# Kernel optimization log

Measured on AMD Instinct MI355X. Metric: run time of the kernel, lower is better.

## Reference

```python
import jax, jax.numpy as jnp
import numpy as np

B, S, D_IN = 4, 2048, 1024
EMBED, HEADS = 1024, 16
HEAD_DIM = EMBED // HEADS


def setup_inputs() -> dict:
    key = jax.random.key(0)
    k1, k2, k3 = jax.random.split(key, 3)
    x = jax.random.normal(k1, (B, S, D_IN), dtype=jnp.float32)
    # xavier-uniform-ish init scales
    lim_qkv = float(np.sqrt(6.0 / (D_IN + 3 * EMBED)))
    lim_o = float(np.sqrt(6.0 / (EMBED + EMBED)))
    w_qkv = jax.random.uniform(k2, (3 * EMBED, D_IN), minval=-lim_qkv, maxval=lim_qkv, dtype=jnp.float32)
    b_qkv = jnp.zeros((3 * EMBED,), dtype=jnp.float32)
    w_o = jax.random.uniform(k3, (EMBED, EMBED), minval=-lim_o, maxval=lim_o, dtype=jnp.float32)
    b_o = jnp.zeros((EMBED,), dtype=jnp.float32)
    return {"x": x, "w_qkv": w_qkv, "b_qkv": b_qkv, "w_o": w_o, "b_o": b_o}


def reference(x, w_qkv, b_qkv, w_o, b_o):
    b, s, _ = x.shape
    qkv = jnp.einsum('bsi,oi->bso', x, w_qkv) + b_qkv            # (b, s, 3E)
    qkv = qkv.reshape(b, s, HEADS, 3 * HEAD_DIM).transpose(0, 2, 1, 3)  # (b, h, s, 3d)
    q, k, v = jnp.split(qkv, 3, axis=-1)                          # each (b, h, s, d)
    scale = 1.0 / jnp.sqrt(jnp.float32(HEAD_DIM))
    attn = jnp.einsum('bhqd,bhkd->bhqk', q, k) * scale            # (b, h, s, s)
    attn = jax.nn.softmax(attn, axis=-1)
    vals = jnp.einsum('bhqk,bhkd->bhqd', attn, v)                 # (b, h, s, d)
    # NOTE: original torch code reshapes (b,h,s,d) -> (b,s,e) WITHOUT transposing
    # heads back; jnp.reshape reproduces that flattening exactly.
    vals = vals.reshape(b, s, EMBED)
    out = jnp.einsum('bse,oe->bso', vals, w_o) + b_o              # (b, s, E)
    return out
```

## Files before the change

### kernel.cpp

```cpp
#include <hip/hip_runtime.h>
#include <stdint.h>
#include <stddef.h>

#define DEVINL __device__ __forceinline__

typedef unsigned short u16;
typedef unsigned int u32;
typedef __attribute__((ext_vector_type(8))) short short8;
typedef __attribute__((ext_vector_type(4))) float f32x4;
typedef __attribute__((ext_vector_type(4))) u32 u32x4;
typedef __attribute__((ext_vector_type(2))) u32 u32x2;

#define QSCALE 0.18033688011112042f

DEVINL u16 f2bf(float f) {
    u32 u = __builtin_bit_cast(u32, f);
    u32 r = (u + 0x7fffu + ((u >> 16) & 1u)) >> 16;
    return (u16)r;
}

DEVINL void gld_lds16(const void* g, void* l) {
    __builtin_amdgcn_global_load_lds(
        (__attribute__((address_space(1))) u32*)(uintptr_t)g,
        (__attribute__((address_space(3))) u32*)l, 16, 0, 0);
}

DEVINL u32 pack_bf16_trunc(float lo, float hi) {
    return __builtin_amdgcn_perm(__builtin_bit_cast(u32, hi),
                                 __builtin_bit_cast(u32, lo), 0x07060302u);
}

__global__ void prep_inputs(const float* __restrict__ x, const float* __restrict__ wqkv,
                            const float* __restrict__ bqkv, const float* __restrict__ wo,
                            u16* __restrict__ xb, u16* __restrict__ wqb,
                            u16* __restrict__ wob, float* __restrict__ bsc) {
    int blk = blockIdx.x;
    if (blk < 6144) {
        const float* src; u16* dst; int base; bool qscale = false;
        if (blk < 4096)      { src = x;    dst = xb;  base = blk; }
        else if (blk < 5632) { src = wqkv; dst = wqb; base = blk - 4096; qscale = true; }
        else                 { src = wo;   dst = wob; base = blk - 5632; }
        int i = (base * 256 + threadIdx.x) * 8;
        float sc = 1.0f;
        if (qscale) { int row = i >> 10; if ((row % 192) < 64) sc = QSCALE; }
        float4 a = *(const float4*)(src + i);
        float4 c = *(const float4*)(src + i + 4);
        union { u16 s[8]; u32x4 v; } t;
        t.s[0] = f2bf(a.x * sc); t.s[1] = f2bf(a.y * sc); t.s[2] = f2bf(a.z * sc); t.s[3] = f2bf(a.w * sc);
        t.s[4] = f2bf(c.x * sc); t.s[5] = f2bf(c.y * sc); t.s[6] = f2bf(c.z * sc); t.s[7] = f2bf(c.w * sc);
        *(u32x4*)(dst + i) = t.v;
    } else {
        int i = (blk - 6144) * 256 + threadIdx.x;
        float sc = ((i % 192) < 64) ? QSCALE : 1.0f;
        bsc[i] = bqkv[i] * sc;
    }
}

__global__ void gemm_qkv(const u16* __restrict__ A, const u16* __restrict__ Bm,
                         const float* __restrict__ bias, u16* __restrict__ qkvb,
                         u16* __restrict__ vtb) {
    const int K = 1024, N = 3072;
    __shared__ u16 As[128 * 32];
    __shared__ u16 Bs[128 * 32];
    const int tid = threadIdx.x;
    const int lane = tid & 63;
    const int wv = tid >> 6, wr = wv >> 1, wc = wv & 1;
    const int l15 = lane & 15, quad = lane >> 4;
    const int m0 = blockIdx.y * 128, n0 = blockIdx.x * 128;

    f32x4 acc[4][4];
#pragma unroll
    for (int i = 0; i < 4; i++)
#pragma unroll
        for (int j = 0; j < 4; j++) acc[i][j] = (f32x4){0.f, 0.f, 0.f, 0.f};

    const u16* Ab = A + (size_t)m0 * K;
    const u16* Bb = Bm + (size_t)n0 * K;
    const int srow = tid >> 2;
    const int sc8 = (tid & 3) * 8;

    for (int k0 = 0; k0 < K; k0 += 32) {
#pragma unroll
        for (int i = 0; i < 2; i++) {
            int row = i * 64 + srow;
            gld_lds16(Ab + (size_t)row * K + k0 + sc8, (char*)As + (size_t)(i * 256 + tid) * 16);
            gld_lds16(Bb + (size_t)row * K + k0 + sc8, (char*)Bs + (size_t)(i * 256 + tid) * 16);
        }
        __syncthreads();
        short8 af[4], bf8[4];
#pragma unroll
        for (int mi = 0; mi < 4; mi++)
            af[mi] = *(const short8*)(As + (wr * 64 + mi * 16 + l15) * 32 + quad * 8);
#pragma unroll
        for (int ni = 0; ni < 4; ni++)
            bf8[ni] = *(const short8*)(Bs + (wc * 64 + ni * 16 + l15) * 32 + quad * 8);
#pragma unroll
        for (int mi = 0; mi < 4; mi++)
#pragma unroll
            for (int ni = 0; ni < 4; ni++)
                acc[mi][ni] = __builtin_amdgcn_mfma_f32_16x16x32_bf16(af[mi], bf8[ni], acc[mi][ni], 0, 0, 0);
        __syncthreads();
    }

#pragma unroll
    for (int mi = 0; mi < 4; mi++) {
        int row_b = m0 + wr * 64 + mi * 16 + quad * 4;
#pragma unroll
        for (int ni = 0; ni < 4; ni++) {
            int c0 = n0 + wc * 64 + ni * 16;
            int sec0 = c0 % 192;
            float bv = bias[c0 + l15];
            float v0 = acc[mi][ni][0] + bv;
            float v1 = acc[mi][ni][1] + bv;
            float v2 = acc[mi][ni][2] + bv;
            float v3 = acc[mi][ni][3] + bv;
            if (sec0 >= 128) {
                int hh = c0 / 192;
                int b = row_b >> 11;
                int s = row_b & 2047;
                int d = sec0 - 128 + l15;
                u32 lo = (u32)f2bf(v0) | ((u32)f2bf(v1) << 16);
                u32 hi = (u32)f2bf(v2) | ((u32)f2bf(v3) << 16);
                *(u32x2*)(vtb + ((size_t)((b * 16 + hh) * 64 + d)) * 2048 + s) = (u32x2){lo, hi};
            } else {
                int col = c0 + l15;
                qkvb[(size_t)(row_b + 0) * N + col] = f2bf(v0);
                qkvb[(size_t)(row_b + 1) * N + col] = f2bf(v1);
                qkvb[(size_t)(row_b + 2) * N + col] = f2bf(v2);
                qkvb[(size_t)(row_b + 3) * N + col] = f2bf(v3);
            }
        }
    }
}

__global__ void gemm_out(const u16* __restrict__ A, const u16* __restrict__ Bm,
                         const float* __restrict__ bias, float* __restrict__ C) {
    const int K = 1024, N = 1024;
    __shared__ u16 As[128 * 32];
    __shared__ u16 Bs[64 * 32];
    const int tid = threadIdx.x;
    const int lane = tid & 63;
    const int wv = tid >> 6, wr = wv >> 1, wc = wv & 1;
    const int l15 = lane & 15, quad = lane >> 4;
    const int m0 = blockIdx.y * 128, n0 = blockIdx.x * 64;

    f32x4 acc[4][2];
#pragma unroll
    for (int i = 0; i < 4; i++)
#pragma unroll
        for (int j = 0; j < 2; j++) acc[i][j] = (f32x4){0.f, 0.f, 0.f, 0.f};

    const u16* Ab = A + (size_t)m0 * K;
    const u16* Bb = Bm + (size_t)n0 * K;
    const int srow = tid >> 2;
    const int sc8 = (tid & 3) * 8;

    for (int k0 = 0; k0 < K; k0 += 32) {
#pragma unroll
        for (int i = 0; i < 2; i++)
            gld_lds16(Ab + (size_t)(i * 64 + srow) * K + k0 + sc8, (char*)As + (size_t)(i * 256 + tid) * 16);
        gld_lds16(Bb + (size_t)srow * K + k0 + sc8, (char*)Bs + (size_t)tid * 16);
        __syncthreads();
        short8 af[4], bf8[2];
#pragma unroll
        for (int mi = 0; mi < 4; mi++)
            af[mi] = *(const short8*)(As + (wr * 64 + mi * 16 + l15) * 32 + quad * 8);
#pragma unroll
        for (int ni = 0; ni < 2; ni++)
            bf8[ni] = *(const short8*)(Bs + (wc * 32 + ni * 16 + l15) * 32 + quad * 8);
#pragma unroll
        for (int mi = 0; mi < 4; mi++)
#pragma unroll
            for (int ni = 0; ni < 2; ni++)
                acc[mi][ni] = __builtin_amdgcn_mfma_f32_16x16x32_bf16(af[mi], bf8[ni], acc[mi][ni], 0, 0, 0);
        __syncthreads();
    }

#pragma unroll
    for (int mi = 0; mi < 4; mi++) {
        int row_b = m0 + wr * 64 + mi * 16 + quad * 4;
#pragma unroll
        for (int ni = 0; ni < 2; ni++) {
            int col = n0 + wc * 32 + ni * 16 + l15;
            float bv = bias[col];
#pragma unroll
            for (int r = 0; r < 4; r++)
                C[(size_t)(row_b + r) * N + col] = acc[mi][ni][r] + bv;
        }
    }
}

__launch_bounds__(256, 4)
__global__ void flash_attn(const u16* __restrict__ qkv, const u16* __restrict__ vt,
                           u16* __restrict__ vals2) {
    __shared__ u16 Ks[64 * 72];
    __shared__ u16 Vts[64 * 72];
    __shared__ u16 Ps[4][32 * 72];

    const int tid = threadIdx.x;
    const int lane = tid & 63, wv = tid >> 6;
    const int l15 = lane & 15, quad = lane >> 4;
    const int s0 = blockIdx.x * 128;
    const int bh = blockIdx.y, b = bh >> 4, h = bh & 15;

    short8 qf[2][2];
    const u16* qbase = qkv + (size_t)(b * 2048 + s0 + wv * 32) * 3072 + h * 192;
#pragma unroll
    for (int qi = 0; qi < 2; qi++)
#pragma unroll
        for (int ks = 0; ks < 2; ks++)
            qf[qi][ks] = *(const short8*)(qbase + (size_t)(qi * 16 + l15) * 3072 + ks * 32 + quad * 8);

    f32x4 o_acc[2][4];
    f32x4 sum_acc[2];
#pragma unroll
    for (int qi = 0; qi < 2; qi++) {
        sum_acc[qi] = (f32x4){0.f, 0.f, 0.f, 0.f};
#pragma unroll
        for (int nd = 0; nd < 4; nd++) o_acc[qi][nd] = (f32x4){0.f, 0.f, 0.f, 0.f};
    }

    const u16* kg = qkv + (size_t)(b * 2048) * 3072 + h * 192 + 64;
    const u16* vg = vt + (size_t)bh * 64 * 2048;
    const int srow = tid >> 2;
    const int sc16 = (tid & 3) * 16;

    const short8 ones = (short8){0x3F80, 0x3F80, 0x3F80, 0x3F80, 0x3F80, 0x3F80, 0x3F80, 0x3F80};

    for (int kb = 0; kb < 2048; kb += 64) {
        __syncthreads();
        u32x4 k0 = *(const u32x4*)(kg + (size_t)(kb + srow) * 3072 + sc16);
        u32x4 k1 = *(const u32x4*)(kg + (size_t)(kb + srow) * 3072 + sc16 + 8);
        u32x4 v0 = *(const u32x4*)(vg + (size_t)srow * 2048 + kb + sc16);
        u32x4 v1 = *(const u32x4*)(vg + (size_t)srow * 2048 + kb + sc16 + 8);
        *(u32x4*)(Ks + srow * 72 + sc16) = k0;
        *(u32x4*)(Ks + srow * 72 + sc16 + 8) = k1;
        *(u32x4*)(Vts + srow * 72 + sc16) = v0;
        *(u32x4*)(Vts + srow * 72 + sc16 + 8) = v1;
        __syncthreads();

        f32x4 s_acc[4][2];
#pragma unroll
        for (int ki = 0; ki < 4; ki++)
#pragma unroll
            for (int qi = 0; qi < 2; qi++) s_acc[ki][qi] = (f32x4){0.f, 0.f, 0.f, 0.f};
#pragma unroll
        for (int ki = 0; ki < 4; ki++) {
#pragma unroll
            for (int ks = 0; ks < 2; ks++) {
                short8 kf = *(const short8*)(Ks + (ki * 16 + l15) * 72 + ks * 32 + quad * 8);
#pragma unroll
                for (int qi = 0; qi < 2; qi++)
                    s_acc[ki][qi] = __builtin_amdgcn_mfma_f32_16x16x32_bf16(kf, qf[qi][ks], s_acc[ki][qi], 0, 0, 0);
            }
        }

#pragma unroll
        for (int ki = 0; ki < 4; ki++)
#pragma unroll
            for (int qi = 0; qi < 2; qi++) {
                float p0 = __builtin_amdgcn_exp2f(s_acc[ki][qi][0]);
                float p1 = __builtin_amdgcn_exp2f(s_acc[ki][qi][1]);
                float p2 = __builtin_amdgcn_exp2f(s_acc[ki][qi][2]);
                float p3 = __builtin_amdgcn_exp2f(s_acc[ki][qi][3]);
                u32x2 pk = (u32x2){pack_bf16_trunc(p0, p1), pack_bf16_trunc(p2, p3)};
                *(u32x2*)(Ps[wv] + (qi * 16 + l15) * 72 + ki * 16 + quad * 4) = pk;
            }

#pragma unroll
        for (int c = 0; c < 2; c++) {
            short8 ap[2];
#pragma unroll
            for (int qi = 0; qi < 2; qi++)
                ap[qi] = *(const short8*)(Ps[wv] + (qi * 16 + l15) * 72 + c * 32 + quad * 8);
#pragma unroll
            for (int qi = 0; qi < 2; qi++)
                sum_acc[qi] = __builtin_amdgcn_mfma_f32_16x16x32_bf16(ap[qi], ones, sum_acc[qi], 0, 0, 0);
#pragma unroll
            for (int nd = 0; nd < 4; nd++) {
                short8 bv = *(const short8*)(Vts + (nd * 16 + l15) * 72 + c * 32 + quad * 8);
#pragma unroll
                for (int qi = 0; qi < 2; qi++)
                    o_acc[qi][nd] = __builtin_amdgcn_mfma_f32_16x16x32_bf16(ap[qi], bv, o_acc[qi][nd], 0, 0, 0);
            }
        }
    }

#pragma unroll
    for (int qi = 0; qi < 2; qi++) {
        f32x4 inv;
#pragma unroll
        for (int r = 0; r < 4; r++) inv[r] = 1.0f / sum_acc[qi][r];
#pragma unroll
        for (int nd = 0; nd < 4; nd++) {
            int d = nd * 16 + l15;
#pragma unroll
            for (int r = 0; r < 4; r++) {
                int s = s0 + wv * 32 + qi * 16 + quad * 4 + r;
                size_t row2 = (size_t)(b * 2048 + h * 128 + (s >> 4));
                int col2 = ((s & 15) << 6) + d;
                vals2[row2 * 1024 + col2] = f2bf(o_acc[qi][nd][r] * inv[r]);
            }
        }
    }
}

extern "C" void kernel_launch(void* const* d_in, const int* in_sizes, int n_in,
                              void* d_out, int out_size, void* d_ws, size_t ws_size,
                              hipStream_t stream) {
    (void)in_sizes; (void)n_in; (void)out_size; (void)ws_size;
    const float* x      = (const float*)d_in[0];
    const float* w_qkv  = (const float*)d_in[1];
    const float* b_qkv  = (const float*)d_in[2];
    const float* w_o    = (const float*)d_in[3];
    const float* b_o    = (const float*)d_in[4];
    float* out = (float*)d_out;

    char* ws = (char*)d_ws;
    u16* xb   = (u16*)(ws);
    u16* wqb  = (u16*)(ws + 16777216);
    u16* wob  = (u16*)(ws + 23068672);
    u16* qkvb = (u16*)(ws + 25165824);
    u16* vtb  = (u16*)(ws + 75497472);
    u16* v2b  = (u16*)(ws + 92274688);
    float* bsc = (float*)(ws + 92274688);

    prep_inputs<<<6156, 256, 0, stream>>>(x, w_qkv, b_qkv, w_o, xb, wqb, wob, bsc);

    gemm_qkv<<<dim3(24, 64), 256, 0, stream>>>(xb, wqb, bsc, qkvb, vtb);

    flash_attn<<<dim3(16, 64), 256, 0, stream>>>(qkvb, vtb, v2b);

    gemm_out<<<dim3(16, 64), 256, 0, stream>>>(v2b, wob, b_o, out);
}
```

Baseline: 274.5 us.

## Split flash attention waves across query and key halves with cross-wave reduction

Each block now processes 128 keys per iteration. Waves are arranged as 2 query groups × 2 key halves, and each wave handles 64 queries against 64 keys, so every K/V fragment read from LDS feeds twice as many MFMAs. At the end, the partial O and row sums from the two key-half waves are combined through shared memory before normalisation. The cost is a larger register footprint (launch bounds drop from 4 to 2 blocks per CU), more LDS per block, and an extra reduction step.

```diff
diff --git a/kernel.cpp b/kernel.cpp
--- a/kernel.cpp
+++ b/kernel.cpp
@@ -190,31 +190,33 @@
     }
 }
 
-__launch_bounds__(256, 4)
+__launch_bounds__(256, 2)
 __global__ void flash_attn(const u16* __restrict__ qkv, const u16* __restrict__ vt,
                            u16* __restrict__ vals2) {
-    __shared__ u16 Ks[64 * 72];
-    __shared__ u16 Vts[64 * 72];
-    __shared__ u16 Ps[4][32 * 72];
+    __shared__ u16 SM[36352];
+    u16* Ks  = SM;
+    u16* Vts = SM + 9216;
+    u16* Ps  = SM + 17920;
 
     const int tid = threadIdx.x;
     const int lane = tid & 63, wv = tid >> 6;
+    const int qw = wv >> 1, kw = wv & 1;
     const int l15 = lane & 15, quad = lane >> 4;
     const int s0 = blockIdx.x * 128;
     const int bh = blockIdx.y, b = bh >> 4, h = bh & 15;
 
-    short8 qf[2][2];
-    const u16* qbase = qkv + (size_t)(b * 2048 + s0 + wv * 32) * 3072 + h * 192;
-#pragma unroll
-    for (int qi = 0; qi < 2; qi++)
+    short8 qf[4][2];
+    const u16* qbase = qkv + (size_t)(b * 2048 + s0 + qw * 64) * 3072 + h * 192;
+#pragma unroll
+    for (int qi = 0; qi < 4; qi++)
 #pragma unroll
         for (int ks = 0; ks < 2; ks++)
             qf[qi][ks] = *(const short8*)(qbase + (size_t)(qi * 16 + l15) * 3072 + ks * 32 + quad * 8);
 
-    f32x4 o_acc[2][4];
-    f32x4 sum_acc[2];
-#pragma unroll
-    for (int qi = 0; qi < 2; qi++) {
+    f32x4 o_acc[4][4];
+    f32x4 sum_acc[4];
+#pragma unroll
+    for (int qi = 0; qi < 4; qi++) {
         sum_acc[qi] = (f32x4){0.f, 0.f, 0.f, 0.f};
 #pragma unroll
         for (int nd = 0; nd < 4; nd++) o_acc[qi][nd] = (f32x4){0.f, 0.f, 0.f, 0.f};
@@ -222,35 +224,45 @@
 
     const u16* kg = qkv + (size_t)(b * 2048) * 3072 + h * 192 + 64;
     const u16* vg = vt + (size_t)bh * 64 * 2048;
-    const int srow = tid >> 2;
-    const int sc16 = (tid & 3) * 16;
-
+
+    const int krow = tid >> 1, khalf = (tid & 1) * 32;
+    const int vrow = tid >> 2, vq4 = (tid & 3) * 32;
+
+    u16* Pw = Ps + wv * 64 * 72;
     const short8 ones = (short8){0x3F80, 0x3F80, 0x3F80, 0x3F80, 0x3F80, 0x3F80, 0x3F80, 0x3F80};
 
-    for (int kb = 0; kb < 2048; kb += 64) {
-        __syncthreads();
-        u32x4 k0 = *(const u32x4*)(kg + (size_t)(kb + srow) * 3072 + sc16);
-        u32x4 k1 = *(const u32x4*)(kg + (size_t)(kb + srow) * 3072 + sc16 + 8);
-        u32x4 v0 = *(const u32x4*)(vg + (size_t)srow * 2048 + kb + sc16);
-        u32x4 v1 = *(const u32x4*)(vg + (size_t)srow * 2048 + kb + sc16 + 8);
-        *(u32x4*)(Ks + srow * 72 + sc16) = k0;
-        *(u32x4*)(Ks + srow * 72 + sc16 + 8) = k1;
-        *(u32x4*)(Vts + srow * 72 + sc16) = v0;
-        *(u32x4*)(Vts + srow * 72 + sc16 + 8) = v1;
-        __syncthreads();
-
-        f32x4 s_acc[4][2];
+    for (int kb = 0; kb < 2048; kb += 128) {
+        __syncthreads();
+        const u16* kgr = kg + (size_t)(kb + krow) * 3072 + khalf;
+        const u16* vgr = vg + (size_t)vrow * 2048 + kb + vq4;
+        u32x4 ka = *(const u32x4*)(kgr);
+        u32x4 kb4 = *(const u32x4*)(kgr + 8);
+        u32x4 kc = *(const u32x4*)(kgr + 16);
+        u32x4 kd = *(const u32x4*)(kgr + 24);
+        u32x4 va = *(const u32x4*)(vgr);
+        u32x4 vb4 = *(const u32x4*)(vgr + 8);
+        u32x4 vc = *(const u32x4*)(vgr + 16);
+        u32x4 vd = *(const u32x4*)(vgr + 24);
+        u16* kdst = Ks + krow * 72 + khalf;
+        u16* vdst = Vts + vrow * 136 + vq4;
+        *(u32x4*)(kdst) = ka;  *(u32x4*)(kdst + 8) = kb4;
+        *(u32x4*)(kdst + 16) = kc; *(u32x4*)(kdst + 24) = kd;
+        *(u32x4*)(vdst) = va;  *(u32x4*)(vdst + 8) = vb4;
+        *(u32x4*)(vdst + 16) = vc; *(u32x4*)(vdst + 24) = vd;
+        __syncthreads();
+
+        f32x4 s_acc[4][4];
 #pragma unroll
         for (int ki = 0; ki < 4; ki++)
 #pragma unroll
-            for (int qi = 0; qi < 2; qi++) s_acc[ki][qi] = (f32x4){0.f, 0.f, 0.f, 0.f};
+            for (int qi = 0; qi < 4; qi++) s_acc[ki][qi] = (f32x4){0.f, 0.f, 0.f, 0.f};
 #pragma unroll
         for (int ki = 0; ki < 4; ki++) {
 #pragma unroll
             for (int ks = 0; ks < 2; ks++) {
-                short8 kf = *(const short8*)(Ks + (ki * 16 + l15) * 72 + ks * 32 + quad * 8);
-#pragma unroll
-                for (int qi = 0; qi < 2; qi++)
+                short8 kf = *(const short8*)(Ks + (kw * 64 + ki * 16 + l15) * 72 + ks * 32 + quad * 8);
+#pragma unroll
+                for (int qi = 0; qi < 4; qi++)
                     s_acc[ki][qi] = __builtin_amdgcn_mfma_f32_16x16x32_bf16(kf, qf[qi][ks], s_acc[ki][qi], 0, 0, 0);
             }
         }
@@ -258,48 +270,65 @@
 #pragma unroll
         for (int ki = 0; ki < 4; ki++)
 #pragma unroll
-            for (int qi = 0; qi < 2; qi++) {
+            for (int qi = 0; qi < 4; qi++) {
                 float p0 = __builtin_amdgcn_exp2f(s_acc[ki][qi][0]);
                 float p1 = __builtin_amdgcn_exp2f(s_acc[ki][qi][1]);
                 float p2 = __builtin_amdgcn_exp2f(s_acc[ki][qi][2]);
                 float p3 = __builtin_amdgcn_exp2f(s_acc[ki][qi][3]);
                 u32x2 pk = (u32x2){pack_bf16_trunc(p0, p1), pack_bf16_trunc(p2, p3)};
-                *(u32x2*)(Ps[wv] + (qi * 16 + l15) * 72 + ki * 16 + quad * 4) = pk;
+                *(u32x2*)(Pw + (qi * 16 + l15) * 72 + ki * 16 + quad * 4) = pk;
             }
 
 #pragma unroll
         for (int c = 0; c < 2; c++) {
-            short8 ap[2];
-#pragma unroll
-            for (int qi = 0; qi < 2; qi++)
-                ap[qi] = *(const short8*)(Ps[wv] + (qi * 16 + l15) * 72 + c * 32 + quad * 8);
-#pragma unroll
-            for (int qi = 0; qi < 2; qi++)
+            short8 ap[4];
+#pragma unroll
+            for (int qi = 0; qi < 4; qi++)
+                ap[qi] = *(const short8*)(Pw + (qi * 16 + l15) * 72 + c * 32 + quad * 8);
+#pragma unroll
+            for (int qi = 0; qi < 4; qi++)
                 sum_acc[qi] = __builtin_amdgcn_mfma_f32_16x16x32_bf16(ap[qi], ones, sum_acc[qi], 0, 0, 0);
 #pragma unroll
             for (int nd = 0; nd < 4; nd++) {
-                short8 bv = *(const short8*)(Vts + (nd * 16 + l15) * 72 + c * 32 + quad * 8);
-#pragma unroll
-                for (int qi = 0; qi < 2; qi++)
+                short8 bv = *(const short8*)(Vts + (nd * 16 + l15) * 136 + kw * 64 + c * 32 + quad * 8);
+#pragma unroll
+                for (int qi = 0; qi < 4; qi++)
                     o_acc[qi][nd] = __builtin_amdgcn_mfma_f32_16x16x32_bf16(ap[qi], bv, o_acc[qi][nd], 0, 0, 0);
             }
         }
     }
 
-#pragma unroll
-    for (int qi = 0; qi < 2; qi++) {
-        f32x4 inv;
-#pragma unroll
-        for (int r = 0; r < 4; r++) inv[r] = 1.0f / sum_acc[qi][r];
-#pragma unroll
-        for (int nd = 0; nd < 4; nd++) {
-            int d = nd * 16 + l15;
-#pragma unroll
-            for (int r = 0; r < 4; r++) {
-                int s = s0 + wv * 32 + qi * 16 + quad * 4 + r;
-                size_t row2 = (size_t)(b * 2048 + h * 128 + (s >> 4));
-                int col2 = ((s & 15) << 6) + d;
-                vals2[row2 * 1024 + col2] = f2bf(o_acc[qi][nd][r] * inv[r]);
+    float* Ored = (float*)SM;
+    float* Sred = (float*)Ps;
+    __syncthreads();
+    if (kw == 1) {
+#pragma unroll
+        for (int qi = 0; qi < 4; qi++) {
+#pragma unroll
+            for (int nd = 0; nd < 4; nd++)
+                *(f32x4*)(Ored + (((qw * 16 + qi * 4 + nd) * 64) + lane) * 4) = o_acc[qi][nd];
+            *(f32x4*)(Sred + (((qw * 4 + qi) * 64) + lane) * 4) = sum_acc[qi];
+        }
+    }
+    __syncthreads();
+    if (kw == 0) {
+#pragma unroll
+        for (int qi = 0; qi < 4; qi++) {
+            f32x4 sp = *(const f32x4*)(Sred + (((qw * 4 + qi) * 64) + lane) * 4);
+            f32x4 inv;
+#pragma unroll
+            for (int r = 0; r < 4; r++) inv[r] = 1.0f / (sum_acc[qi][r] + sp[r]);
+#pragma unroll
+            for (int nd = 0; nd < 4; nd++) {
+                f32x4 op = *(const f32x4*)(Ored + (((qw * 16 + qi * 4 + nd) * 64) + lane) * 4);
+                int d = nd * 16 + l15;
+#pragma unroll
+                for (int r = 0; r < 4; r++) {
+                    int s = s0 + qw * 64 + qi * 16 + quad * 4 + r;
+                    size_t row2 = (size_t)(b * 2048 + h * 128 + (s >> 4));
+                    int col2 = ((s & 15) << 6) + d;
+                    vals2[row2 * 1024 + col2] = f2bf((o_acc[qi][nd][r] + op[r]) * inv[r]);
+                }
             }
         }
     }
```

After: 290.7 us. +5.9%, slower.
